# Performance work log

Hardware: AMD Instinct MI355X
Metric: run time of the kernel (lower is better)

## Reference

```python
import jax, jax.numpy as jnp
import numpy as np

B, NI, NA, D = 16, 2048, 2048, 256

def setup_inputs() -> dict:
    key = jax.random.key(0)
    k1, k2, k3 = jax.random.split(key, 3)
    input_seq = jax.random.normal(k1, (B, NI, D), dtype=jnp.float32)
    attendee_seq = jax.random.normal(k2, (B, NA, D), dtype=jnp.float32)
    # glorot-ish scale for bilinear weight
    W = jax.random.normal(k3, (D, D), dtype=jnp.float32) * (1.0 / np.sqrt(D))
    return {"input_seq": input_seq, "attendee_seq": attendee_seq, "W": W}

def reference(input_seq, attendee_seq, W):
    # bilinear scores: (x_i W) . a_j   -> [B, NI, NA]
    xW = jnp.einsum('bid,de->bie', input_seq, W)
    scores = jnp.einsum('bie,bje->bij', xW, attendee_seq)
    A = jax.nn.softmax(scores, axis=2)                 # softmax over attendee axis
    # weighted context: sum_j A[b,i,j] * v[b,j,:] -> [B, NI, D]
    attended = jnp.einsum('bij,bjd->bid', A, attendee_seq)
    return attended
```

## Files before the change

### kernel.cpp

```cpp
#include <hip/hip_runtime.h>
#include <hip/hip_bf16.h>

#define BB 16
#define NI 2048
#define NA 2048
#define DD 256
#define KVB 32
#define NT (NA / KVB)

typedef _Float16 half8 __attribute__((ext_vector_type(8)));
typedef __attribute__((ext_vector_type(16))) float f32x16;
typedef __attribute__((ext_vector_type(4))) unsigned int uint4v;

typedef const unsigned int CGU __attribute__((address_space(1)));
typedef unsigned int LU __attribute__((address_space(3)));

static __device__ __forceinline__ unsigned short f2h(float f) {
  union { _Float16 h; unsigned short u; } x; x.h = (_Float16)f; return x.u;
}
static __device__ __forceinline__ float h2f(unsigned short u) {
  union { _Float16 h; unsigned short u; } x; x.u = u; return (float)x.h;
}
static __device__ __forceinline__ unsigned int pk2(float a, float b) {
  return __builtin_bit_cast(unsigned int, __builtin_amdgcn_cvt_pkrtz(a, b));
}
static __device__ __forceinline__ float ex2(float x) {
  return __builtin_amdgcn_exp2f(x);
}
static __device__ __forceinline__ void gload16(const unsigned short* g, unsigned short* l) {
  __builtin_amdgcn_global_load_lds((CGU*)g, (LU*)l, 16, 0, 0);
}

__global__ void prep_kernel(const float* __restrict__ a,
                            unsigned short* __restrict__ kfrag,
                            unsigned short* __restrict__ vfrag,
                            const float* __restrict__ w,
                            unsigned short* __restrict__ wth,
                            unsigned short* __restrict__ wtl) {
  __shared__ float t[64][65];
  int bx = blockIdx.x;
  int tid = threadIdx.x;
  int rr = tid >> 4, c4 = tid & 15;

  if (bx >= 2048) {
    int r = bx - 2048;
    int dt = r >> 2, et = r & 3;
    int d0 = dt * 64, e0 = et * 64;
    int cc = c4 * 4;
#pragma unroll
    for (int k = 0; k < 4; ++k) {
      int row = rr + k * 16;
      float4 v = *(const float4*)(w + (size_t)(d0 + row) * DD + e0 + cc);
      t[row][cc + 0] = v.x; t[row][cc + 1] = v.y; t[row][cc + 2] = v.z; t[row][cc + 3] = v.w;
    }
    __syncthreads();
#pragma unroll
    for (int k = 0; k < 4; ++k) {
      int e = rr + k * 16;
      int eg = e0 + e;
      ushort4 h, l;
      float v0 = t[cc + 0][e]; h.x = f2h(v0); l.x = f2h(v0 - h2f(h.x));
      float v1 = t[cc + 1][e]; h.y = f2h(v1); l.y = f2h(v1 - h2f(h.y));
      float v2 = t[cc + 2][e]; h.z = f2h(v2); l.z = f2h(v2 - h2f(h.z));
      float v3 = t[cc + 3][e]; h.w = f2h(v3); l.w = f2h(v3 - h2f(h.w));
      int dd = d0 + cc;
      int u = dd >> 3, sub = dd & 7;
      size_t off = (size_t)eg * DD + ((u ^ (eg & 7)) * 8) + sub;
      *(ushort4*)(wth + off) = h;
      *(ushort4*)(wtl + off) = l;
    }
    return;
  }

  int b = bx >> 7;
  int r = bx & 127;
  int jt_t = r >> 2, dt_t = r & 3;
  int j0 = jt_t * 64, d0 = dt_t * 64;
#pragma unroll
  for (int k = 0; k < 4; ++k) {
    int row = rr + k * 16;
    int j = j0 + row;
    int d = d0 + c4 * 4;
    float4 v = *(const float4*)(a + ((size_t)b * NA + j) * DD + d);
    ushort4 hh;
    hh.x = f2h(v.x); hh.y = f2h(v.y); hh.z = f2h(v.z); hh.w = f2h(v.w);
    int kt = j >> 5;
    int ks = d >> 4;
    int lk = (j & 31) + 32 * ((d >> 3) & 1);
    *(ushort4*)(kfrag + (((size_t)b * NT + kt) * 16 + ks) * 512 + lk * 8 + (c4 & 1) * 4) = hh;
    t[row][c4 * 4 + 0] = v.x; t[row][c4 * 4 + 1] = v.y;
    t[row][c4 * 4 + 2] = v.z; t[row][c4 * 4 + 3] = v.w;
  }
  __syncthreads();
#pragma unroll
  for (int k = 0; k < 4; ++k) {
    int dl = rr + k * 16;
    int d = d0 + dl;
    int j = j0 + c4 * 4;
    ushort4 o;
    o.x = f2h(t[c4 * 4 + 0][dl]); o.y = f2h(t[c4 * 4 + 1][dl]);
    o.z = f2h(t[c4 * 4 + 2][dl]); o.w = f2h(t[c4 * 4 + 3][dl]);
    int kt = j >> 5;
    int hi = c4 & 1;
    int m = (c4 >> 2) & 1;
    int ebase = ((c4 >> 1) & 1) * 4;
    int hh_ = d >> 7, dtl = (d >> 5) & 3;
    int lv = (d & 31) + 32 * hi;
    *(ushort4*)(vfrag + ((((((size_t)b * NT + kt) * 2 + hh_) * 4 + dtl) * 2 + m) * 512) + lv * 8 + ebase) = o;
  }
}

__global__ __launch_bounds__(256, 2) void qgemm_kernel(
    const float* __restrict__ x, const unsigned short* __restrict__ wth,
    const unsigned short* __restrict__ wtl, unsigned short* __restrict__ qf) {
  __shared__ unsigned short wb[2][64 * 256];
  const int tid = threadIdx.x;
  const int lane = tid & 63;
  const int wv = tid >> 6;
  const int quad = lane >> 4;
  const int l16 = lane & 15;
  const int m0 = blockIdx.x * 64;

  half8 xf[8];
  {
    const float* xr = x + (size_t)(m0 + wv * 16 + l16) * DD;
#pragma unroll
    for (int c = 0; c < 8; ++c) {
      float4 a = *(const float4*)(xr + c * 32 + quad * 8);
      float4 b = *(const float4*)(xr + c * 32 + quad * 8 + 4);
      half8 v;
      v[0] = (_Float16)a.x; v[1] = (_Float16)a.y; v[2] = (_Float16)a.z; v[3] = (_Float16)a.w;
      v[4] = (_Float16)b.x; v[5] = (_Float16)b.y; v[6] = (_Float16)b.z; v[7] = (_Float16)b.w;
      xf[c] = v;
    }
  }

#pragma unroll 1
  for (int eg = 0; eg < 4; ++eg) {
    uint4 t0[8], t1[8];
    {
      const unsigned short* sh = wth + (size_t)(eg * 64) * DD;
      const unsigned short* sl = wtl + (size_t)(eg * 64) * DD;
#pragma unroll
      for (int i = 0; i < 8; ++i) {
        t0[i] = *(const uint4*)(sh + (i * 256 + tid) * 8);
        t1[i] = *(const uint4*)(sl + (i * 256 + tid) * 8);
      }
    }
    __syncthreads();
#pragma unroll
    for (int i = 0; i < 8; ++i) {
      *(uint4*)(wb[0] + (i * 256 + tid) * 8) = t0[i];
      *(uint4*)(wb[1] + (i * 256 + tid) * 8) = t1[i];
    }
    __syncthreads();
#pragma unroll
    for (int etl = 0; etl < 4; ++etl) {
      int rloc = etl * 16 + l16;
      float4 acc4 = make_float4(0.f, 0.f, 0.f, 0.f);
      typedef __attribute__((ext_vector_type(4))) float f32x4;
      f32x4 acc; acc[0] = acc[1] = acc[2] = acc[3] = 0.f;
#pragma unroll
      for (int c = 0; c < 8; ++c) {
        int off = rloc * DD + (((4 * c + quad) ^ (rloc & 7)) * 8);
        half8 wh = *(const half8*)(wb[0] + off);
        half8 wl = *(const half8*)(wb[1] + off);
        acc = __builtin_amdgcn_mfma_f32_16x16x32_f16(xf[c], wh, acc, 0, 0, 0);
        acc = __builtin_amdgcn_mfma_f32_16x16x32_f16(xf[c], wl, acc, 0, 0, 0);
      }
      (void)acc4;
      int e = eg * 64 + etl * 16 + l16;
#pragma unroll
      for (int rg = 0; rg < 4; ++rg) {
        qf[(size_t)(m0 + wv * 16 + 4 * quad + rg) * DD + e] = f2h(acc[rg] * 1.44269504f);
      }
    }
  }
}

__global__ __launch_bounds__(256, 2) void attn_kernel(
    const unsigned short* __restrict__ kfrag, const unsigned short* __restrict__ vfrag,
    const unsigned short* __restrict__ qf, float* __restrict__ out) {
  __shared__ unsigned short kls[2][KVB * DD];

  const int tid = threadIdx.x;
  const int lane = tid & 63;
  const int wv = tid >> 6;
  const int pr = wv >> 1;
  const int h = wv & 1;
  const int l31 = lane & 31;
  const int hi = lane >> 5;

  int bx = blockIdx.x;
  int lbx = (bx & 7) * 64 + (bx >> 3);
  const int b = lbx >> 5;
  const int qbase = (lbx & 31) * 64 + pr * 32;

  const unsigned short* kfb = kfrag + (size_t)b * NT * 8192;

  half8 qh[16];
  {
    const unsigned short* qr = qf + ((size_t)b * NI + qbase + l31) * DD + hi * 8;
#pragma unroll
    for (int ks = 0; ks < 16; ++ks)
      qh[ks] = *(const half8*)(qr + ks * 16);
  }

  f32x16 acc[4];
#pragma unroll
  for (int dt = 0; dt < 4; ++dt)
#pragma unroll
    for (int i = 0; i < 16; ++i) acc[dt][i] = 0.f;
  float m0r = -INFINITY;
  float l0 = 0.f;

  const unsigned short* vp = vfrag + (((size_t)b * NT * 2 + h) * 4) * 1024 + lane * 8;
  const unsigned short* sp = kfb + 8192 + (wv * 512 + lane * 8);

#pragma unroll
  for (int i = 0; i < 4; ++i) {
    int off = (i * 4 + wv) * 512;
    gload16(kfb + off + lane * 8, &kls[0][off]);
  }
  __syncthreads();

#pragma unroll 1
  for (int kt = 0; kt < NT; ++kt) {
    half8 vb[8];
#pragma unroll
    for (int i = 0; i < 8; ++i)
      vb[i] = *(const half8*)(vp + i * 512);

    if (kt + 1 < NT) {
      unsigned short* d = &kls[(kt + 1) & 1][wv * 512];
      gload16(sp + 0 * 2048, d + 0 * 2048);
      gload16(sp + 1 * 2048, d + 1 * 2048);
      gload16(sp + 2 * 2048, d + 2 * 2048);
      gload16(sp + 3 * 2048, d + 3 * 2048);
    }

    const unsigned short* kb = &kls[kt & 1][0];
    f32x16 sA, sB;
#pragma unroll
    for (int i = 0; i < 16; ++i) { sA[i] = 0.f; sB[i] = 0.f; }
    __builtin_amdgcn_s_setprio(1);
#pragma unroll
    for (int ks = 0; ks < 8; ++ks) {
      half8 ka = *(const half8*)(kb + ks * 512 + lane * 8);
      sA = __builtin_amdgcn_mfma_f32_32x32x16_f16(ka, qh[ks], sA, 0, 0, 0);
    }
#pragma unroll
    for (int ks = 8; ks < 16; ++ks) {
      half8 ka = *(const half8*)(kb + ks * 512 + lane * 8);
      sB = __builtin_amdgcn_mfma_f32_32x32x16_f16(ka, qh[ks], sB, 0, 0, 0);
    }
    __builtin_amdgcn_s_setprio(0);
    float p[16];
#pragma unroll
    for (int i = 0; i < 16; ++i) p[i] = sA[i] + sB[i];

    float mt = p[0];
#pragma unroll
    for (int i = 1; i < 16; ++i) mt = fmaxf(mt, p[i]);
    mt = fmaxf(mt, __shfl_xor(mt, 32));
    if (__any(mt > m0r + 11.5416f)) {
      float mn = fmaxf(m0r, mt);
      float sc = ex2(m0r - mn);
      l0 *= sc;
#pragma unroll
      for (int dt = 0; dt < 4; ++dt)
#pragma unroll
        for (int i = 0; i < 16; ++i) acc[dt][i] *= sc;
      m0r = mn;
    }

#pragma unroll
    for (int i = 0; i < 16; ++i) p[i] = ex2(p[i] - m0r);
    float s0 = ((p[0] + p[1]) + (p[2] + p[3])) + ((p[4] + p[5]) + (p[6] + p[7]));
    float s1 = ((p[8] + p[9]) + (p[10] + p[11])) + ((p[12] + p[13]) + (p[14] + p[15]));
    l0 += s0 + s1;

    half8 pa0, pa1;
    {
      uint4v u0 = { pk2(p[0], p[1]), pk2(p[2], p[3]), pk2(p[4], p[5]), pk2(p[6], p[7]) };
      uint4v u1 = { pk2(p[8], p[9]), pk2(p[10], p[11]), pk2(p[12], p[13]), pk2(p[14], p[15]) };
      pa0 = __builtin_bit_cast(half8, u0);
      pa1 = __builtin_bit_cast(half8, u1);
    }

    __builtin_amdgcn_s_setprio(1);
#pragma unroll
    for (int dt = 0; dt < 4; ++dt) {
      acc[dt] = __builtin_amdgcn_mfma_f32_32x32x16_f16(vb[dt * 2 + 0], pa0, acc[dt], 0, 0, 0);
      acc[dt] = __builtin_amdgcn_mfma_f32_32x32x16_f16(vb[dt * 2 + 1], pa1, acc[dt], 0, 0, 0);
    }
    __builtin_amdgcn_s_setprio(0);

    vp += 8192;
    sp += 8192;
    __syncthreads();
  }

  l0 += __shfl_xor(l0, 32);
  float inv0 = 1.0f / l0;
  float* ob = out + ((size_t)b * NI + qbase + l31) * DD + h * 128 + hi * 4;
#pragma unroll
  for (int dt = 0; dt < 4; ++dt) {
#pragma unroll
    for (int rq = 0; rq < 4; ++rq) {
      float4 v;
      v.x = acc[dt][rq * 4 + 0] * inv0;
      v.y = acc[dt][rq * 4 + 1] * inv0;
      v.z = acc[dt][rq * 4 + 2] * inv0;
      v.w = acc[dt][rq * 4 + 3] * inv0;
      *(float4*)(ob + dt * 32 + rq * 8) = v;
    }
  }
}

extern "C" void kernel_launch(void* const* d_in, const int* in_sizes, int n_in,
                              void* d_out, int out_size, void* d_ws, size_t ws_size,
                              hipStream_t stream) {
  const float* x = (const float*)d_in[0];
  const float* att = (const float*)d_in[1];
  const float* W = (const float*)d_in[2];
  float* out = (float*)d_out;

  const size_t NE = (size_t)BB * NA * DD;
  unsigned short* w0    = (unsigned short*)d_ws;
  unsigned short* kfrag = w0;
  unsigned short* vfrag = w0 + NE;
  unsigned short* qfp   = w0 + 2 * NE;
  unsigned short* wth   = w0 + 3 * NE;
  unsigned short* wtl   = w0 + 3 * NE + (size_t)DD * DD;

  prep_kernel<<<2064, 256, 0, stream>>>(att, kfrag, vfrag, W, wth, wtl);
  qgemm_kernel<<<512, 256, 0, stream>>>(x, wth, wtl, qfp);
  attn_kernel<<<512, 256, 0, stream>>>(kfrag, vfrag, qfp, out);
}
```

Baseline: 182.7 us.

## Process two KV tiles per loop iteration with a doubled LDS K buffer

Unrolls the attention main loop so each iteration handles two 32-row KV tiles. K is staged into an LDS buffer twice as large, and both tiles' P·V MFMAs are batched at the end of the iteration. When the running max rises on the second tile, the first tile's fp16 probabilities are rescaled. The aim is to halve the barriers and loop overhead per KV tile and give more independent MFMA work between syncs. The cost is higher LDS use (64KB per block) and more VGPRs for the second V fragment set, which may reduce occupancy or cause spills.

```diff
diff --git a/kernel.cpp b/kernel.cpp
--- a/kernel.cpp
+++ b/kernel.cpp
@@ -7,6 +7,7 @@
 #define DD 256
 #define KVB 32
 #define NT (NA / KVB)
+#define NT2 (NT / 2)
 
 typedef _Float16 half8 __attribute__((ext_vector_type(8)));
 typedef __attribute__((ext_vector_type(16))) float f32x16;
@@ -157,7 +158,6 @@
 #pragma unroll
     for (int etl = 0; etl < 4; ++etl) {
       int rloc = etl * 16 + l16;
-      float4 acc4 = make_float4(0.f, 0.f, 0.f, 0.f);
       typedef __attribute__((ext_vector_type(4))) float f32x4;
       f32x4 acc; acc[0] = acc[1] = acc[2] = acc[3] = 0.f;
 #pragma unroll
@@ -168,7 +168,6 @@
         acc = __builtin_amdgcn_mfma_f32_16x16x32_f16(xf[c], wh, acc, 0, 0, 0);
         acc = __builtin_amdgcn_mfma_f32_16x16x32_f16(xf[c], wl, acc, 0, 0, 0);
       }
-      (void)acc4;
       int e = eg * 64 + etl * 16 + l16;
 #pragma unroll
       for (int rg = 0; rg < 4; ++rg) {
@@ -181,7 +180,7 @@
 __global__ __launch_bounds__(256, 2) void attn_kernel(
     const unsigned short* __restrict__ kfrag, const unsigned short* __restrict__ vfrag,
     const unsigned short* __restrict__ qf, float* __restrict__ out) {
-  __shared__ unsigned short kls[2][KVB * DD];
+  __shared__ unsigned short kls[2][2 * KVB * DD];
 
   const int tid = threadIdx.x;
   const int lane = tid & 63;
@@ -214,44 +213,46 @@
   float m0r = -INFINITY;
   float l0 = 0.f;
 
-  const unsigned short* vp = vfrag + (((size_t)b * NT * 2 + h) * 4) * 1024 + lane * 8;
-  const unsigned short* sp = kfb + 8192 + (wv * 512 + lane * 8);
-
-#pragma unroll
-  for (int i = 0; i < 4; ++i) {
+  const unsigned short* vbase = vfrag + (size_t)b * NT * 8192 + h * 4096 + lane * 8;
+  const unsigned short* sp = kfb + 16384 + (wv * 512 + lane * 8);
+
+#pragma unroll
+  for (int i = 0; i < 8; ++i) {
     int off = (i * 4 + wv) * 512;
     gload16(kfb + off + lane * 8, &kls[0][off]);
   }
   __syncthreads();
 
 #pragma unroll 1
-  for (int kt = 0; kt < NT; ++kt) {
-    half8 vb[8];
-#pragma unroll
-    for (int i = 0; i < 8; ++i)
-      vb[i] = *(const half8*)(vp + i * 512);
-
-    if (kt + 1 < NT) {
-      unsigned short* d = &kls[(kt + 1) & 1][wv * 512];
-      gload16(sp + 0 * 2048, d + 0 * 2048);
-      gload16(sp + 1 * 2048, d + 1 * 2048);
-      gload16(sp + 2 * 2048, d + 2 * 2048);
-      gload16(sp + 3 * 2048, d + 3 * 2048);
-    }
-
-    const unsigned short* kb = &kls[kt & 1][0];
+  for (int kt2 = 0; kt2 < NT2; ++kt2) {
+    const unsigned short* vp0 = vbase;
+    const unsigned short* vp0b = vbase + 2048;
+    half8 vb0[8];
+#pragma unroll
+    for (int i = 0; i < 4; ++i) vb0[i] = *(const half8*)(vp0 + i * 512);
+#pragma unroll
+    for (int i = 0; i < 4; ++i) vb0[4 + i] = *(const half8*)(vp0b + i * 512);
+
+    if (kt2 + 1 < NT2) {
+      unsigned short* d = &kls[(kt2 + 1) & 1][wv * 512];
+#pragma unroll
+      for (int i = 0; i < 8; ++i)
+        gload16(sp + i * 2048, d + i * 2048);
+    }
+
+    const unsigned short* kb0 = &kls[kt2 & 1][0];
     f32x16 sA, sB;
 #pragma unroll
     for (int i = 0; i < 16; ++i) { sA[i] = 0.f; sB[i] = 0.f; }
     __builtin_amdgcn_s_setprio(1);
 #pragma unroll
     for (int ks = 0; ks < 8; ++ks) {
-      half8 ka = *(const half8*)(kb + ks * 512 + lane * 8);
+      half8 ka = *(const half8*)(kb0 + ks * 512 + lane * 8);
       sA = __builtin_amdgcn_mfma_f32_32x32x16_f16(ka, qh[ks], sA, 0, 0, 0);
     }
 #pragma unroll
     for (int ks = 8; ks < 16; ++ks) {
-      half8 ka = *(const half8*)(kb + ks * 512 + lane * 8);
+      half8 ka = *(const half8*)(kb0 + ks * 512 + lane * 8);
       sB = __builtin_amdgcn_mfma_f32_32x32x16_f16(ka, qh[ks], sB, 0, 0, 0);
     }
     __builtin_amdgcn_s_setprio(0);
@@ -273,31 +274,85 @@
         for (int i = 0; i < 16; ++i) acc[dt][i] *= sc;
       m0r = mn;
     }
-
 #pragma unroll
     for (int i = 0; i < 16; ++i) p[i] = ex2(p[i] - m0r);
-    float s0 = ((p[0] + p[1]) + (p[2] + p[3])) + ((p[4] + p[5]) + (p[6] + p[7]));
-    float s1 = ((p[8] + p[9]) + (p[10] + p[11])) + ((p[12] + p[13]) + (p[14] + p[15]));
-    l0 += s0 + s1;
-
-    half8 pa0, pa1;
+    l0 += (((p[0] + p[1]) + (p[2] + p[3])) + ((p[4] + p[5]) + (p[6] + p[7]))) +
+          (((p[8] + p[9]) + (p[10] + p[11])) + ((p[12] + p[13]) + (p[14] + p[15])));
+    half8 pa00, pa01;
     {
       uint4v u0 = { pk2(p[0], p[1]), pk2(p[2], p[3]), pk2(p[4], p[5]), pk2(p[6], p[7]) };
       uint4v u1 = { pk2(p[8], p[9]), pk2(p[10], p[11]), pk2(p[12], p[13]), pk2(p[14], p[15]) };
-      pa0 = __builtin_bit_cast(half8, u0);
-      pa1 = __builtin_bit_cast(half8, u1);
-    }
-
+      pa00 = __builtin_bit_cast(half8, u0);
+      pa01 = __builtin_bit_cast(half8, u1);
+    }
+
+    const unsigned short* vp1 = vbase + 8192;
+    const unsigned short* vp1b = vbase + 10240;
+    half8 vb1[8];
+#pragma unroll
+    for (int i = 0; i < 4; ++i) vb1[i] = *(const half8*)(vp1 + i * 512);
+#pragma unroll
+    for (int i = 0; i < 4; ++i) vb1[4 + i] = *(const half8*)(vp1b + i * 512);
+
+    const unsigned short* kb1 = &kls[kt2 & 1][8192];
+#pragma unroll
+    for (int i = 0; i < 16; ++i) { sA[i] = 0.f; sB[i] = 0.f; }
     __builtin_amdgcn_s_setprio(1);
 #pragma unroll
+    for (int ks = 0; ks < 8; ++ks) {
+      half8 ka = *(const half8*)(kb1 + ks * 512 + lane * 8);
+      sA = __builtin_amdgcn_mfma_f32_32x32x16_f16(ka, qh[ks], sA, 0, 0, 0);
+    }
+#pragma unroll
+    for (int ks = 8; ks < 16; ++ks) {
+      half8 ka = *(const half8*)(kb1 + ks * 512 + lane * 8);
+      sB = __builtin_amdgcn_mfma_f32_32x32x16_f16(ka, qh[ks], sB, 0, 0, 0);
+    }
+    __builtin_amdgcn_s_setprio(0);
+#pragma unroll
+    for (int i = 0; i < 16; ++i) p[i] = sA[i] + sB[i];
+
+    mt = p[0];
+#pragma unroll
+    for (int i = 1; i < 16; ++i) mt = fmaxf(mt, p[i]);
+    mt = fmaxf(mt, __shfl_xor(mt, 32));
+    if (__any(mt > m0r + 11.5416f)) {
+      float mn = fmaxf(m0r, mt);
+      float sc = ex2(m0r - mn);
+      l0 *= sc;
+#pragma unroll
+      for (int dt = 0; dt < 4; ++dt)
+#pragma unroll
+        for (int i = 0; i < 16; ++i) acc[dt][i] *= sc;
+      _Float16 sh = (_Float16)sc;
+      half8 sv = { sh, sh, sh, sh, sh, sh, sh, sh };
+      pa00 *= sv; pa01 *= sv;
+      m0r = mn;
+    }
+#pragma unroll
+    for (int i = 0; i < 16; ++i) p[i] = ex2(p[i] - m0r);
+    l0 += (((p[0] + p[1]) + (p[2] + p[3])) + ((p[4] + p[5]) + (p[6] + p[7]))) +
+          (((p[8] + p[9]) + (p[10] + p[11])) + ((p[12] + p[13]) + (p[14] + p[15])));
+    half8 pa10, pa11;
+    {
+      uint4v u0 = { pk2(p[0], p[1]), pk2(p[2], p[3]), pk2(p[4], p[5]), pk2(p[6], p[7]) };
+      uint4v u1 = { pk2(p[8], p[9]), pk2(p[10], p[11]), pk2(p[12], p[13]), pk2(p[14], p[15]) };
+      pa10 = __builtin_bit_cast(half8, u0);
+      pa11 = __builtin_bit_cast(half8, u1);
+    }
+
+    __builtin_amdgcn_s_setprio(1);
+#pragma unroll
     for (int dt = 0; dt < 4; ++dt) {
-      acc[dt] = __builtin_amdgcn_mfma_f32_32x32x16_f16(vb[dt * 2 + 0], pa0, acc[dt], 0, 0, 0);
-      acc[dt] = __builtin_amdgcn_mfma_f32_32x32x16_f16(vb[dt * 2 + 1], pa1, acc[dt], 0, 0, 0);
+      acc[dt] = __builtin_amdgcn_mfma_f32_32x32x16_f16(vb0[dt * 2 + 0], pa00, acc[dt], 0, 0, 0);
+      acc[dt] = __builtin_amdgcn_mfma_f32_32x32x16_f16(vb0[dt * 2 + 1], pa01, acc[dt], 0, 0, 0);
+      acc[dt] = __builtin_amdgcn_mfma_f32_32x32x16_f16(vb1[dt * 2 + 0], pa10, acc[dt], 0, 0, 0);
+      acc[dt] = __builtin_amdgcn_mfma_f32_32x32x16_f16(vb1[dt * 2 + 1], pa11, acc[dt], 0, 0, 0);
     }
     __builtin_amdgcn_s_setprio(0);
 
-    vp += 8192;
-    sp += 8192;
+    vbase += 16384;
+    sp += 16384;
     __syncthreads();
   }
 
```

Measured after the change: 183.4 us. About the same (+0.4%).

## Software-pipeline QK scores one tile ahead of softmax and PV

Applied to the files above, without the earlier changes.

Computes the QK^T score MFMAs for tile kt+1 before the softmax and PV work of tile kt, with a prologue that computes tile 0 and prefetches tile 1 into the second LDS buffer. The K prefetch now lands two tiles ahead into the buffer just consumed. The goal is to overlap the exp/max VALU work with independent MFMAs so the matrix units do not stall behind the softmax. This keeps an extra set of 32 score accumulators live, which raises register pressure under launch_bounds(256,2). It also tightens the LDS reuse ordering around the single barrier per iteration.

```diff
diff --git a/kernel.cpp b/kernel.cpp
--- a/kernel.cpp
+++ b/kernel.cpp
@@ -157,7 +157,6 @@
 #pragma unroll
     for (int etl = 0; etl < 4; ++etl) {
       int rloc = etl * 16 + l16;
-      float4 acc4 = make_float4(0.f, 0.f, 0.f, 0.f);
       typedef __attribute__((ext_vector_type(4))) float f32x4;
       f32x4 acc; acc[0] = acc[1] = acc[2] = acc[3] = 0.f;
 #pragma unroll
@@ -168,7 +167,6 @@
         acc = __builtin_amdgcn_mfma_f32_16x16x32_f16(xf[c], wh, acc, 0, 0, 0);
         acc = __builtin_amdgcn_mfma_f32_16x16x32_f16(xf[c], wl, acc, 0, 0, 0);
       }
-      (void)acc4;
       int e = eg * 64 + etl * 16 + l16;
 #pragma unroll
       for (int rg = 0; rg < 4; ++rg) {
@@ -215,7 +213,7 @@
   float l0 = 0.f;
 
   const unsigned short* vp = vfrag + (((size_t)b * NT * 2 + h) * 4) * 1024 + lane * 8;
-  const unsigned short* sp = kfb + 8192 + (wv * 512 + lane * 8);
+  const unsigned short* sp = kfb + 16384 + (wv * 512 + lane * 8);
 
 #pragma unroll
   for (int i = 0; i < 4; ++i) {
@@ -223,6 +221,30 @@
     gload16(kfb + off + lane * 8, &kls[0][off]);
   }
   __syncthreads();
+#pragma unroll
+  for (int i = 0; i < 4; ++i) {
+    int off = (i * 4 + wv) * 512;
+    gload16(kfb + 8192 + off + lane * 8, &kls[1][off]);
+  }
+  float p[16];
+  {
+    f32x16 sA, sB;
+#pragma unroll
+    for (int i = 0; i < 16; ++i) { sA[i] = 0.f; sB[i] = 0.f; }
+#pragma unroll
+    for (int ks = 0; ks < 8; ++ks) {
+      half8 ka = *(const half8*)(&kls[0][ks * 512] + lane * 8);
+      sA = __builtin_amdgcn_mfma_f32_32x32x16_f16(ka, qh[ks], sA, 0, 0, 0);
+    }
+#pragma unroll
+    for (int ks = 8; ks < 16; ++ks) {
+      half8 ka = *(const half8*)(&kls[0][ks * 512] + lane * 8);
+      sB = __builtin_amdgcn_mfma_f32_32x32x16_f16(ka, qh[ks], sB, 0, 0, 0);
+    }
+#pragma unroll
+    for (int i = 0; i < 16; ++i) p[i] = sA[i] + sB[i];
+  }
+  __syncthreads();
 
 #pragma unroll 1
   for (int kt = 0; kt < NT; ++kt) {
@@ -231,33 +253,32 @@
     for (int i = 0; i < 8; ++i)
       vb[i] = *(const half8*)(vp + i * 512);
 
-    if (kt + 1 < NT) {
-      unsigned short* d = &kls[(kt + 1) & 1][wv * 512];
+    if (kt + 2 < NT) {
+      unsigned short* d = &kls[kt & 1][wv * 512];
       gload16(sp + 0 * 2048, d + 0 * 2048);
       gload16(sp + 1 * 2048, d + 1 * 2048);
       gload16(sp + 2 * 2048, d + 2 * 2048);
       gload16(sp + 3 * 2048, d + 3 * 2048);
     }
 
-    const unsigned short* kb = &kls[kt & 1][0];
     f32x16 sA, sB;
-#pragma unroll
-    for (int i = 0; i < 16; ++i) { sA[i] = 0.f; sB[i] = 0.f; }
-    __builtin_amdgcn_s_setprio(1);
-#pragma unroll
-    for (int ks = 0; ks < 8; ++ks) {
-      half8 ka = *(const half8*)(kb + ks * 512 + lane * 8);
-      sA = __builtin_amdgcn_mfma_f32_32x32x16_f16(ka, qh[ks], sA, 0, 0, 0);
-    }
-#pragma unroll
-    for (int ks = 8; ks < 16; ++ks) {
-      half8 ka = *(const half8*)(kb + ks * 512 + lane * 8);
-      sB = __builtin_amdgcn_mfma_f32_32x32x16_f16(ka, qh[ks], sB, 0, 0, 0);
-    }
-    __builtin_amdgcn_s_setprio(0);
-    float p[16];
-#pragma unroll
-    for (int i = 0; i < 16; ++i) p[i] = sA[i] + sB[i];
+    if (kt + 1 < NT) {
+      const unsigned short* kb = &kls[(kt + 1) & 1][0];
+#pragma unroll
+      for (int i = 0; i < 16; ++i) { sA[i] = 0.f; sB[i] = 0.f; }
+      __builtin_amdgcn_s_setprio(1);
+#pragma unroll
+      for (int ks = 0; ks < 8; ++ks) {
+        half8 ka = *(const half8*)(kb + ks * 512 + lane * 8);
+        sA = __builtin_amdgcn_mfma_f32_32x32x16_f16(ka, qh[ks], sA, 0, 0, 0);
+      }
+#pragma unroll
+      for (int ks = 8; ks < 16; ++ks) {
+        half8 ka = *(const half8*)(kb + ks * 512 + lane * 8);
+        sB = __builtin_amdgcn_mfma_f32_32x32x16_f16(ka, qh[ks], sB, 0, 0, 0);
+      }
+      __builtin_amdgcn_s_setprio(0);
+    }
 
     float mt = p[0];
 #pragma unroll
@@ -273,13 +294,10 @@
         for (int i = 0; i < 16; ++i) acc[dt][i] *= sc;
       m0r = mn;
     }
-
 #pragma unroll
     for (int i = 0; i < 16; ++i) p[i] = ex2(p[i] - m0r);
-    float s0 = ((p[0] + p[1]) + (p[2] + p[3])) + ((p[4] + p[5]) + (p[6] + p[7]));
-    float s1 = ((p[8] + p[9]) + (p[10] + p[11])) + ((p[12] + p[13]) + (p[14] + p[15]));
-    l0 += s0 + s1;
-
+    l0 += (((p[0] + p[1]) + (p[2] + p[3])) + ((p[4] + p[5]) + (p[6] + p[7]))) +
+          (((p[8] + p[9]) + (p[10] + p[11])) + ((p[12] + p[13]) + (p[14] + p[15])));
     half8 pa0, pa1;
     {
       uint4v u0 = { pk2(p[0], p[1]), pk2(p[2], p[3]), pk2(p[4], p[5]), pk2(p[6], p[7]) };
@@ -295,6 +313,11 @@
       acc[dt] = __builtin_amdgcn_mfma_f32_32x32x16_f16(vb[dt * 2 + 1], pa1, acc[dt], 0, 0, 0);
     }
     __builtin_amdgcn_s_setprio(0);
+
+    if (kt + 1 < NT) {
+#pragma unroll
+      for (int i = 0; i < 16; ++i) p[i] = sA[i] + sB[i];
+    }
 
     vp += 8192;
     sp += 8192;
```

After: 184.6 us. About the same (+1.0%).

## Store W and Q in MFMA fragment order and drop LDS staging in qgemm

Applied to the files above, without the earlier changes.

W's hi/lo fp16 split is now written in per-lane MFMA fragment order, so qgemm loads B operands straight from global memory with no LDS staging or barriers. That lets occupancy be raised to 8 blocks. qgemm now writes Q in the fragment layout the attention kernel consumes, so attn loads Q with lane-contiguous 16-byte reads. The trade is more global/L2 traffic in qgemm in exchange for removing the syncs and LDS copies.

```diff
diff --git a/kernel.cpp b/kernel.cpp
--- a/kernel.cpp
+++ b/kernel.cpp
@@ -10,6 +10,7 @@
 
 typedef _Float16 half8 __attribute__((ext_vector_type(8)));
 typedef __attribute__((ext_vector_type(16))) float f32x16;
+typedef __attribute__((ext_vector_type(4))) float f32x4;
 typedef __attribute__((ext_vector_type(4))) unsigned int uint4v;
 
 typedef const unsigned int CGU __attribute__((address_space(1)));
@@ -35,8 +36,8 @@
                             unsigned short* __restrict__ kfrag,
                             unsigned short* __restrict__ vfrag,
                             const float* __restrict__ w,
-                            unsigned short* __restrict__ wth,
-                            unsigned short* __restrict__ wtl) {
+                            unsigned short* __restrict__ wbfh,
+                            unsigned short* __restrict__ wbfl) {
   __shared__ float t[64][65];
   int bx = blockIdx.x;
   int tid = threadIdx.x;
@@ -44,8 +45,8 @@
 
   if (bx >= 2048) {
     int r = bx - 2048;
-    int dt = r >> 2, et = r & 3;
-    int d0 = dt * 64, e0 = et * 64;
+    int dt = r >> 2, et4 = r & 3;
+    int d0 = dt * 64, e0 = et4 * 64;
     int cc = c4 * 4;
 #pragma unroll
     for (int k = 0; k < 4; ++k) {
@@ -54,20 +55,22 @@
       t[row][cc + 0] = v.x; t[row][cc + 1] = v.y; t[row][cc + 2] = v.z; t[row][cc + 3] = v.w;
     }
     __syncthreads();
+    int d = d0 + cc;
+    int c = d >> 5;
+    int quad = (d >> 3) & 3;
 #pragma unroll
     for (int k = 0; k < 4; ++k) {
-      int e = rr + k * 16;
-      int eg = e0 + e;
+      int e_local = rr + k * 16;
+      int eg = e0 + e_local;
       ushort4 h, l;
-      float v0 = t[cc + 0][e]; h.x = f2h(v0); l.x = f2h(v0 - h2f(h.x));
-      float v1 = t[cc + 1][e]; h.y = f2h(v1); l.y = f2h(v1 - h2f(h.y));
-      float v2 = t[cc + 2][e]; h.z = f2h(v2); l.z = f2h(v2 - h2f(h.z));
-      float v3 = t[cc + 3][e]; h.w = f2h(v3); l.w = f2h(v3 - h2f(h.w));
-      int dd = d0 + cc;
-      int u = dd >> 3, sub = dd & 7;
-      size_t off = (size_t)eg * DD + ((u ^ (eg & 7)) * 8) + sub;
-      *(ushort4*)(wth + off) = h;
-      *(ushort4*)(wtl + off) = l;
+      float v0 = t[cc + 0][e_local]; h.x = f2h(v0); l.x = f2h(v0 - h2f(h.x));
+      float v1 = t[cc + 1][e_local]; h.y = f2h(v1); l.y = f2h(v1 - h2f(h.y));
+      float v2 = t[cc + 2][e_local]; h.z = f2h(v2); l.z = f2h(v2 - h2f(h.z));
+      float v3 = t[cc + 3][e_local]; h.w = f2h(v3); l.w = f2h(v3 - h2f(h.w));
+      int et = eg >> 4, l16e = eg & 15;
+      size_t off = ((size_t)(et * 8 + c) * 64 + quad * 16 + l16e) * 8 + (c4 & 1) * 4;
+      *(ushort4*)(wbfh + off) = h;
+      *(ushort4*)(wbfl + off) = l;
     }
     return;
   }
@@ -110,10 +113,9 @@
   }
 }
 
-__global__ __launch_bounds__(256, 2) void qgemm_kernel(
-    const float* __restrict__ x, const unsigned short* __restrict__ wth,
-    const unsigned short* __restrict__ wtl, unsigned short* __restrict__ qf) {
-  __shared__ unsigned short wb[2][64 * 256];
+__global__ __launch_bounds__(256, 8) void qgemm_kernel(
+    const float* __restrict__ x, const unsigned short* __restrict__ wbfh,
+    const unsigned short* __restrict__ wbfl, unsigned short* __restrict__ qfrag) {
   const int tid = threadIdx.x;
   const int lane = tid & 63;
   const int wv = tid >> 6;
@@ -135,52 +137,31 @@
     }
   }
 
+  const int sub = l16 & 7;
+  const int khalf = (l16 >> 3) & 1;
 #pragma unroll 1
-  for (int eg = 0; eg < 4; ++eg) {
-    uint4 t0[8], t1[8];
-    {
-      const unsigned short* sh = wth + (size_t)(eg * 64) * DD;
-      const unsigned short* sl = wtl + (size_t)(eg * 64) * DD;
-#pragma unroll
-      for (int i = 0; i < 8; ++i) {
-        t0[i] = *(const uint4*)(sh + (i * 256 + tid) * 8);
-        t1[i] = *(const uint4*)(sl + (i * 256 + tid) * 8);
-      }
-    }
-    __syncthreads();
-#pragma unroll
-    for (int i = 0; i < 8; ++i) {
-      *(uint4*)(wb[0] + (i * 256 + tid) * 8) = t0[i];
-      *(uint4*)(wb[1] + (i * 256 + tid) * 8) = t1[i];
-    }
-    __syncthreads();
-#pragma unroll
-    for (int etl = 0; etl < 4; ++etl) {
-      int rloc = etl * 16 + l16;
-      float4 acc4 = make_float4(0.f, 0.f, 0.f, 0.f);
-      typedef __attribute__((ext_vector_type(4))) float f32x4;
-      f32x4 acc; acc[0] = acc[1] = acc[2] = acc[3] = 0.f;
-#pragma unroll
-      for (int c = 0; c < 8; ++c) {
-        int off = rloc * DD + (((4 * c + quad) ^ (rloc & 7)) * 8);
-        half8 wh = *(const half8*)(wb[0] + off);
-        half8 wl = *(const half8*)(wb[1] + off);
-        acc = __builtin_amdgcn_mfma_f32_16x16x32_f16(xf[c], wh, acc, 0, 0, 0);
-        acc = __builtin_amdgcn_mfma_f32_16x16x32_f16(xf[c], wl, acc, 0, 0, 0);
-      }
-      (void)acc4;
-      int e = eg * 64 + etl * 16 + l16;
-#pragma unroll
-      for (int rg = 0; rg < 4; ++rg) {
-        qf[(size_t)(m0 + wv * 16 + 4 * quad + rg) * DD + e] = f2h(acc[rg] * 1.44269504f);
-      }
+  for (int et = 0; et < 16; ++et) {
+    f32x4 acc; acc[0] = acc[1] = acc[2] = acc[3] = 0.f;
+#pragma unroll
+    for (int c = 0; c < 8; ++c) {
+      half8 wh = *(const half8*)(wbfh + ((size_t)(et * 8 + c) * 64 + lane) * 8);
+      half8 wl = *(const half8*)(wbfl + ((size_t)(et * 8 + c) * 64 + lane) * 8);
+      acc = __builtin_amdgcn_mfma_f32_16x16x32_f16(xf[c], wh, acc, 0, 0, 0);
+      acc = __builtin_amdgcn_mfma_f32_16x16x32_f16(xf[c], wl, acc, 0, 0, 0);
+    }
+#pragma unroll
+    for (int rg = 0; rg < 4; ++rg) {
+      int qrow = m0 + wv * 16 + 4 * quad + rg;
+      int qt = qrow >> 5, l31q = qrow & 31;
+      qfrag[((size_t)(qt * 16 + et)) * 512 + (l31q + 32 * khalf) * 8 + sub] =
+          f2h(acc[rg] * 1.44269504f);
     }
   }
 }
 
 __global__ __launch_bounds__(256, 2) void attn_kernel(
     const unsigned short* __restrict__ kfrag, const unsigned short* __restrict__ vfrag,
-    const unsigned short* __restrict__ qf, float* __restrict__ out) {
+    const unsigned short* __restrict__ qfrag, float* __restrict__ out) {
   __shared__ unsigned short kls[2][KVB * DD];
 
   const int tid = threadIdx.x;
@@ -200,10 +181,10 @@
 
   half8 qh[16];
   {
-    const unsigned short* qr = qf + ((size_t)b * NI + qbase + l31) * DD + hi * 8;
+    const unsigned short* qr = qfrag + ((size_t)((b * NI + qbase) >> 5) * 16) * 512 + lane * 8;
 #pragma unroll
     for (int ks = 0; ks < 16; ++ks)
-      qh[ks] = *(const half8*)(qr + ks * 16);
+      qh[ks] = *(const half8*)(qr + ks * 512);
   }
 
   f32x16 acc[4];
@@ -276,9 +257,8 @@
 
 #pragma unroll
     for (int i = 0; i < 16; ++i) p[i] = ex2(p[i] - m0r);
-    float s0 = ((p[0] + p[1]) + (p[2] + p[3])) + ((p[4] + p[5]) + (p[6] + p[7]));
-    float s1 = ((p[8] + p[9]) + (p[10] + p[11])) + ((p[12] + p[13]) + (p[14] + p[15]));
-    l0 += s0 + s1;
+    l0 += (((p[0] + p[1]) + (p[2] + p[3])) + ((p[4] + p[5]) + (p[6] + p[7]))) +
+          (((p[8] + p[9]) + (p[10] + p[11])) + ((p[12] + p[13]) + (p[14] + p[15])));
 
     half8 pa0, pa1;
     {
@@ -330,11 +310,11 @@
   unsigned short* w0    = (unsigned short*)d_ws;
   unsigned short* kfrag = w0;
   unsigned short* vfrag = w0 + NE;
-  unsigned short* qfp   = w0 + 2 * NE;
-  unsigned short* wth   = w0 + 3 * NE;
-  unsigned short* wtl   = w0 + 3 * NE + (size_t)DD * DD;
-
-  prep_kernel<<<2064, 256, 0, stream>>>(att, kfrag, vfrag, W, wth, wtl);
-  qgemm_kernel<<<512, 256, 0, stream>>>(x, wth, wtl, qfp);
-  attn_kernel<<<512, 256, 0, stream>>>(kfrag, vfrag, qfp, out);
-}
+  unsigned short* qfrag = w0 + 2 * NE;
+  unsigned short* wbfh  = w0 + 3 * NE;
+  unsigned short* wbfl  = w0 + 3 * NE + 65536;
+
+  prep_kernel<<<2064, 256, 0, stream>>>(att, kfrag, vfrag, W, wbfh, wbfl);
+  qgemm_kernel<<<512, 256, 0, stream>>>(x, wbfh, wbfl, qfrag);
+  attn_kernel<<<512, 256, 0, stream>>>(kfrag, vfrag, qfrag, out);
+}
```

Measured after the change: 162.3 us, median of 2. 11.2% less time.
